# Kernel tuning notes

Measured on AMD Instinct MI355X. Metric: run time of the kernel, lower is better.

The kernel has to match this reference:

```python
import jax, jax.numpy as jnp
import numpy as np

N = 4  # hypercomplex dimension

def setup_inputs() -> dict:
    key = jax.random.key(0)
    k1, k2, k3 = jax.random.split(key, 3)
    x = jax.random.normal(k1, (32, 196, 768), dtype=jnp.float32)
    # [n, out_pad/n, in_pad/n] = [4, 3072//4, 768//4]
    weight_components = jax.random.normal(k2, (N, 768, 192), dtype=jnp.float32) * 0.02
    bias = jax.random.normal(k3, (3072,), dtype=jnp.float32) * 0.02
    return {"x": x, "weight_components": weight_components, "bias": bias}

def reference(x, weight_components, bias):
    n, out_blk, in_blk = weight_components.shape
    batch_shape = x.shape[:-1]
    xb = x.reshape(-1, n, in_blk)  # [B, n, in_blk]
    # original: out[:, (i+j)%n] += x[:, j] @ W[i].T
    # equivalently out[:, k] = sum_j x[:, j] @ W[(k-j)%n].T
    k_idx = jnp.arange(n)[:, None]
    j_idx = jnp.arange(n)[None, :]
    Wperm = weight_components[(k_idx - j_idx) % n]  # [n(k), n(j), out_blk, in_blk]
    out = jnp.einsum('bjc,kjoc->bko', xb, Wperm)    # [B, n, out_blk]
    out = out.reshape(-1, n * out_blk) + bias
    return out.reshape(*batch_shape, n * out_blk)
```

## Files before the change

### kernel.cpp

```cpp
#include <hip/hip_runtime.h>
#include <stdint.h>

#define M_ROWS 6272
#define K_DIM  768
#define N_DIM  3072
#define BM 128
#define BN 128
#define BK 32
#define NITER (K_DIM / BK)

#define X_CHUNKS (M_ROWS * K_DIM / 8)
#define W_CHUNKS (N_DIM * K_DIM / 8)
#define X_BLOCKS (X_CHUNKS / 256)
#define W_BLOCKS (W_CHUNKS / 256)

typedef unsigned short u16;
typedef __attribute__((ext_vector_type(8))) __bf16 bf16x8;
typedef __attribute__((ext_vector_type(4))) float f32x4;

__device__ __forceinline__ u16 f32_to_bf16(float f) {
    unsigned u = __float_as_uint(f);
    unsigned r = 0x7FFFu + ((u >> 16) & 1u);
    return (u16)((u + r) >> 16);
}

__device__ __forceinline__ unsigned pack2(float a, float b) {
    return (unsigned)f32_to_bf16(a) | ((unsigned)f32_to_bf16(b) << 16);
}

__global__ void prep_kernel(const float* __restrict__ x, const float* __restrict__ w,
                            u16* __restrict__ xb, u16* __restrict__ wb) {
    int b = blockIdx.x;
    if (b < X_BLOCKS) {
        int idx = b * 256 + threadIdx.x;
        const float4* xp = (const float4*)x + (size_t)idx * 2;
        float4 a = xp[0], c = xp[1];
        uint4 v;
        v.x = pack2(a.x, a.y);
        v.y = pack2(a.z, a.w);
        v.z = pack2(c.x, c.y);
        v.w = pack2(c.z, c.w);
        ((uint4*)xb)[idx] = v;
    } else {
        int idx = (b - X_BLOCKS) * 256 + threadIdx.x;
        int n    = idx / 96;
        int kc   = idx - n * 96;
        int kblk = n / 768;
        int o    = n - kblk * 768;
        int j    = kc / 24;
        int c8   = kc - j * 24;
        int i    = (kblk - j) & 3;
        const float* src = w + (((size_t)i * 768 + o) * 192 + c8 * 8);
        float4 a = ((const float4*)src)[0];
        float4 c = ((const float4*)src)[1];
        uint4 v;
        v.x = pack2(a.x, a.y);
        v.y = pack2(a.z, a.w);
        v.z = pack2(c.x, c.y);
        v.w = pack2(c.z, c.w);
        ((uint4*)wb)[idx] = v;
    }
}

__device__ __forceinline__ void load_lds16(const u16* g, u16* l) {
    __builtin_amdgcn_global_load_lds(
        (const __attribute__((address_space(1))) void*)g,
        (__attribute__((address_space(3))) void*)l, 16, 0, 0);
}

__global__ __launch_bounds__(256) void gemm_bt(
    const u16* __restrict__ A,
    const u16* __restrict__ B,
    const float* __restrict__ bias,
    float* __restrict__ C)
{
    __shared__ u16 As[2][BM * BK];
    __shared__ u16 Bs[2][BN * BK];

    const int tid    = threadIdx.x;
    const int wave   = tid >> 6;
    const int lane   = tid & 63;
    const int lane16 = lane & 15;
    const int quad   = lane >> 4;
    const int wr     = wave >> 1;
    const int wc     = wave & 1;

    const int rowBase = blockIdx.y * BM;
    const int colBase = blockIdx.x * BN;

    const int c0 = tid;
    const int c1 = tid + 256;
    const int r0 = c0 >> 2, s0 = (c0 & 3) ^ ((r0 >> 1) & 3);
    const int r1 = c1 >> 2, s1 = (c1 & 3) ^ ((r1 >> 1) & 3);
    const u16* Ag0 = A + (size_t)(rowBase + r0) * K_DIM + s0 * 8;
    const u16* Ag1 = A + (size_t)(rowBase + r1) * K_DIM + s1 * 8;
    const u16* Bg0 = B + (size_t)(colBase + r0) * K_DIM + s0 * 8;
    const u16* Bg1 = B + (size_t)(colBase + r1) * K_DIM + s1 * 8;
    const int l0 = c0 * 8;
    const int l1 = c1 * 8;

    const int swz  = (lane16 >> 1) & 3;
    const int slot = (quad ^ swz) * 8;
    int aoff[4], boff[4];
#pragma unroll
    for (int i = 0; i < 4; ++i)
        aoff[i] = (wr * 64 + i * 16 + lane16) * BK + slot;
#pragma unroll
    for (int j = 0; j < 4; ++j)
        boff[j] = (wc * 64 + j * 16 + lane16) * BK + slot;

    f32x4 acc[4][4] = {};

    load_lds16(Ag0, &As[0][l0]);
    load_lds16(Ag1, &As[0][l1]);
    load_lds16(Bg0, &Bs[0][l0]);
    load_lds16(Bg1, &Bs[0][l1]);

#pragma unroll 2
    for (int it = 0; it < NITER; ++it) {
        const int cur = it & 1, nxt = cur ^ 1;
        __syncthreads();
        if (it + 1 < NITER) {
            const int k = (it + 1) * BK;
            load_lds16(Ag0 + k, &As[nxt][l0]);
            load_lds16(Ag1 + k, &As[nxt][l1]);
            load_lds16(Bg0 + k, &Bs[nxt][l0]);
            load_lds16(Bg1 + k, &Bs[nxt][l1]);
        }

        bf16x8 af[4], bfv[4];
#pragma unroll
        for (int i = 0; i < 4; ++i)
            af[i] = *(const bf16x8*)&As[cur][aoff[i]];
#pragma unroll
        for (int j = 0; j < 4; ++j)
            bfv[j] = *(const bf16x8*)&Bs[cur][boff[j]];
#pragma unroll
        for (int i = 0; i < 4; ++i)
#pragma unroll
            for (int j = 0; j < 4; ++j)
                acc[i][j] = __builtin_amdgcn_mfma_f32_16x16x32_bf16(
                    af[i], bfv[j], acc[i][j], 0, 0, 0);
    }

    float bv[4];
#pragma unroll
    for (int j = 0; j < 4; ++j)
        bv[j] = bias[colBase + wc * 64 + j * 16 + lane16];
#pragma unroll
    for (int i = 0; i < 4; ++i) {
        int row0 = rowBase + wr * 64 + i * 16 + quad * 4;
#pragma unroll
        for (int r = 0; r < 4; ++r) {
            float* cp = C + (size_t)(row0 + r) * N_DIM + colBase + wc * 64 + lane16;
#pragma unroll
            for (int j = 0; j < 4; ++j)
                cp[j * 16] = acc[i][j][r] + bv[j];
        }
    }
}

extern "C" void kernel_launch(void* const* d_in, const int* in_sizes, int n_in,
                              void* d_out, int out_size, void* d_ws, size_t ws_size,
                              hipStream_t stream) {
    const float* x    = (const float*)d_in[0];
    const float* w    = (const float*)d_in[1];
    const float* bias = (const float*)d_in[2];
    float* out = (float*)d_out;

    u16* xb = (u16*)d_ws;
    u16* wb = (u16*)((char*)d_ws + (size_t)M_ROWS * K_DIM * 2);

    hipLaunchKernelGGL(prep_kernel, dim3(X_BLOCKS + W_BLOCKS), dim3(256),
                       0, stream, x, w, xb, wb);
    hipLaunchKernelGGL(gemm_bt, dim3(N_DIM / BN, M_ROWS / BM), dim3(256),
                       0, stream, xb, wb, bias, out);
}
```

Before: 140.0 us.

## Replace direct global-to-LDS loads with register-staged double-buffered prefetch

Stops using global_load_lds direct-to-LDS copies and instead loads each tile into registers two iterations ahead, writing them into the other LDS buffer after the MFMA block. The main loop is restructured with a prologue and two peeled epilogue iterations, with one barrier per iteration placed after the stores. The aim is to hide global-load latency behind the MFMA work. In exchange it uses more VGPRs and adds an extra LDS write instruction per chunk.

```diff
diff --git a/kernel.cpp b/kernel.cpp
--- a/kernel.cpp
+++ b/kernel.cpp
@@ -62,12 +62,6 @@
     }
 }
 
-__device__ __forceinline__ void load_lds16(const u16* g, u16* l) {
-    __builtin_amdgcn_global_load_lds(
-        (const __attribute__((address_space(1))) void*)g,
-        (__attribute__((address_space(3))) void*)l, 16, 0, 0);
-}
-
 __global__ __launch_bounds__(256) void gemm_bt(
     const u16* __restrict__ A,
     const u16* __restrict__ B,
@@ -92,12 +86,15 @@
     const int c1 = tid + 256;
     const int r0 = c0 >> 2, s0 = (c0 & 3) ^ ((r0 >> 1) & 3);
     const int r1 = c1 >> 2, s1 = (c1 & 3) ^ ((r1 >> 1) & 3);
-    const u16* Ag0 = A + (size_t)(rowBase + r0) * K_DIM + s0 * 8;
-    const u16* Ag1 = A + (size_t)(rowBase + r1) * K_DIM + s1 * 8;
-    const u16* Bg0 = B + (size_t)(colBase + r0) * K_DIM + s0 * 8;
-    const u16* Bg1 = B + (size_t)(colBase + r1) * K_DIM + s1 * 8;
-    const int l0 = c0 * 8;
-    const int l1 = c1 * 8;
+    const uint4* Ag0 = (const uint4*)(A + (size_t)(rowBase + r0) * K_DIM + s0 * 8);
+    const uint4* Ag1 = (const uint4*)(A + (size_t)(rowBase + r1) * K_DIM + s1 * 8);
+    const uint4* Bg0 = (const uint4*)(B + (size_t)(colBase + r0) * K_DIM + s0 * 8);
+    const uint4* Bg1 = (const uint4*)(B + (size_t)(colBase + r1) * K_DIM + s1 * 8);
+    uint4* Al0 = (uint4*)&As[0][c0 * 8];
+    uint4* Al1 = (uint4*)&As[0][c1 * 8];
+    uint4* Bl0 = (uint4*)&Bs[0][c0 * 8];
+    uint4* Bl1 = (uint4*)&Bs[0][c1 * 8];
+    const int bufStride = (BM * BK) / 8;
 
     const int swz  = (lane16 >> 1) & 3;
     const int slot = (quad ^ swz) * 8;
@@ -111,23 +108,60 @@
 
     f32x4 acc[4][4] = {};
 
-    load_lds16(Ag0, &As[0][l0]);
-    load_lds16(Ag1, &As[0][l1]);
-    load_lds16(Bg0, &Bs[0][l0]);
-    load_lds16(Bg1, &Bs[0][l1]);
+    const int kStep = BK / 8;
+
+    uint4 ga0 = Ag0[0], ga1 = Ag1[0], gb0 = Bg0[0], gb1 = Bg1[0];
+    Al0[0] = ga0; Al1[0] = ga1; Bl0[0] = gb0; Bl1[0] = gb1;
+    ga0 = Ag0[kStep]; ga1 = Ag1[kStep]; gb0 = Bg0[kStep]; gb1 = Bg1[kStep];
+    __syncthreads();
 
 #pragma unroll 2
-    for (int it = 0; it < NITER; ++it) {
+    for (int it = 0; it < NITER - 2; ++it) {
         const int cur = it & 1, nxt = cur ^ 1;
+
+        bf16x8 af[4], bfv[4];
+#pragma unroll
+        for (int i = 0; i < 4; ++i)
+            af[i] = *(const bf16x8*)&As[cur][aoff[i]];
+#pragma unroll
+        for (int j = 0; j < 4; ++j)
+            bfv[j] = *(const bf16x8*)&Bs[cur][boff[j]];
+#pragma unroll
+        for (int i = 0; i < 4; ++i)
+#pragma unroll
+            for (int j = 0; j < 4; ++j)
+                acc[i][j] = __builtin_amdgcn_mfma_f32_16x16x32_bf16(
+                    af[i], bfv[j], acc[i][j], 0, 0, 0);
+
+        const int o = nxt * bufStride;
+        Al0[o] = ga0; Al1[o] = ga1; Bl0[o] = gb0; Bl1[o] = gb1;
+        const int g = (it + 2) * kStep;
+        ga0 = Ag0[g]; ga1 = Ag1[g]; gb0 = Bg0[g]; gb1 = Bg1[g];
         __syncthreads();
-        if (it + 1 < NITER) {
-            const int k = (it + 1) * BK;
-            load_lds16(Ag0 + k, &As[nxt][l0]);
-            load_lds16(Ag1 + k, &As[nxt][l1]);
-            load_lds16(Bg0 + k, &Bs[nxt][l0]);
-            load_lds16(Bg1 + k, &Bs[nxt][l1]);
-        }
-
+    }
+
+    {
+        const int cur = (NITER - 2) & 1, nxt = cur ^ 1;
+        bf16x8 af[4], bfv[4];
+#pragma unroll
+        for (int i = 0; i < 4; ++i)
+            af[i] = *(const bf16x8*)&As[cur][aoff[i]];
+#pragma unroll
+        for (int j = 0; j < 4; ++j)
+            bfv[j] = *(const bf16x8*)&Bs[cur][boff[j]];
+#pragma unroll
+        for (int i = 0; i < 4; ++i)
+#pragma unroll
+            for (int j = 0; j < 4; ++j)
+                acc[i][j] = __builtin_amdgcn_mfma_f32_16x16x32_bf16(
+                    af[i], bfv[j], acc[i][j], 0, 0, 0);
+        const int o = nxt * bufStride;
+        Al0[o] = ga0; Al1[o] = ga1; Bl0[o] = gb0; Bl1[o] = gb1;
+        __syncthreads();
+    }
+
+    {
+        const int cur = (NITER - 1) & 1;
         bf16x8 af[4], bfv[4];
 #pragma unroll
         for (int i = 0; i < 4; ++i)
```

Result: faster. 134.9 us (-3.7%).

## Load GEMM operand fragments directly from global memory into registers, bypassing LDS

Applied to the files above, without the earlier changes.

Removes the shared-memory double buffer and block-wide barriers. Each wave loads its A and B MFMA fragments directly from global memory into registers, with one-iteration register prefetch. This cuts LDS traffic and synchronisation but loses intra-block data sharing, doubling global/L2 reads, and the per-lane strided row accesses may coalesce poorly.

```diff
diff --git a/kernel.cpp b/kernel.cpp
--- a/kernel.cpp
+++ b/kernel.cpp
@@ -4,10 +4,7 @@
 #define M_ROWS 6272
 #define K_DIM  768
 #define N_DIM  3072
-#define BM 128
-#define BN 128
-#define BK 32
-#define NITER (K_DIM / BK)
+#define NITER (K_DIM / 32)
 
 #define X_CHUNKS (M_ROWS * K_DIM / 8)
 #define W_CHUNKS (N_DIM * K_DIM / 8)
@@ -62,21 +59,12 @@
     }
 }
 
-__device__ __forceinline__ void load_lds16(const u16* g, u16* l) {
-    __builtin_amdgcn_global_load_lds(
-        (const __attribute__((address_space(1))) void*)g,
-        (__attribute__((address_space(3))) void*)l, 16, 0, 0);
-}
-
 __global__ __launch_bounds__(256) void gemm_bt(
     const u16* __restrict__ A,
     const u16* __restrict__ B,
     const float* __restrict__ bias,
     float* __restrict__ C)
 {
-    __shared__ u16 As[2][BM * BK];
-    __shared__ u16 Bs[2][BN * BK];
-
     const int tid    = threadIdx.x;
     const int wave   = tid >> 6;
     const int lane   = tid & 63;
@@ -85,74 +73,55 @@
     const int wr     = wave >> 1;
     const int wc     = wave & 1;
 
-    const int rowBase = blockIdx.y * BM;
-    const int colBase = blockIdx.x * BN;
+    const int rowBase = blockIdx.y * 128 + wr * 64;
+    const int colBase = blockIdx.x * 128 + wc * 64;
 
-    const int c0 = tid;
-    const int c1 = tid + 256;
-    const int r0 = c0 >> 2, s0 = (c0 & 3) ^ ((r0 >> 1) & 3);
-    const int r1 = c1 >> 2, s1 = (c1 & 3) ^ ((r1 >> 1) & 3);
-    const u16* Ag0 = A + (size_t)(rowBase + r0) * K_DIM + s0 * 8;
-    const u16* Ag1 = A + (size_t)(rowBase + r1) * K_DIM + s1 * 8;
-    const u16* Bg0 = B + (size_t)(colBase + r0) * K_DIM + s0 * 8;
-    const u16* Bg1 = B + (size_t)(colBase + r1) * K_DIM + s1 * 8;
-    const int l0 = c0 * 8;
-    const int l1 = c1 * 8;
-
-    const int swz  = (lane16 >> 1) & 3;
-    const int slot = (quad ^ swz) * 8;
-    int aoff[4], boff[4];
+    const u16* ap[4];
+    const u16* bp[4];
 #pragma unroll
     for (int i = 0; i < 4; ++i)
-        aoff[i] = (wr * 64 + i * 16 + lane16) * BK + slot;
+        ap[i] = A + (size_t)(rowBase + i * 16 + lane16) * K_DIM + quad * 8;
 #pragma unroll
     for (int j = 0; j < 4; ++j)
-        boff[j] = (wc * 64 + j * 16 + lane16) * BK + slot;
+        bp[j] = B + (size_t)(colBase + j * 16 + lane16) * K_DIM + quad * 8;
 
     f32x4 acc[4][4] = {};
 
-    load_lds16(Ag0, &As[0][l0]);
-    load_lds16(Ag1, &As[0][l1]);
-    load_lds16(Bg0, &Bs[0][l0]);
-    load_lds16(Bg1, &Bs[0][l1]);
+    bf16x8 a0[4], b0[4], a1[4], b1[4];
+#pragma unroll
+    for (int i = 0; i < 4; ++i) a0[i] = *(const bf16x8*)(ap[i]);
+#pragma unroll
+    for (int j = 0; j < 4; ++j) b0[j] = *(const bf16x8*)(bp[j]);
 
 #pragma unroll 2
     for (int it = 0; it < NITER; ++it) {
-        const int cur = it & 1, nxt = cur ^ 1;
-        __syncthreads();
         if (it + 1 < NITER) {
-            const int k = (it + 1) * BK;
-            load_lds16(Ag0 + k, &As[nxt][l0]);
-            load_lds16(Ag1 + k, &As[nxt][l1]);
-            load_lds16(Bg0 + k, &Bs[nxt][l0]);
-            load_lds16(Bg1 + k, &Bs[nxt][l1]);
+            const int k = (it + 1) * 32;
+#pragma unroll
+            for (int i = 0; i < 4; ++i) a1[i] = *(const bf16x8*)(ap[i] + k);
+#pragma unroll
+            for (int j = 0; j < 4; ++j) b1[j] = *(const bf16x8*)(bp[j] + k);
         }
-
-        bf16x8 af[4], bfv[4];
-#pragma unroll
-        for (int i = 0; i < 4; ++i)
-            af[i] = *(const bf16x8*)&As[cur][aoff[i]];
-#pragma unroll
-        for (int j = 0; j < 4; ++j)
-            bfv[j] = *(const bf16x8*)&Bs[cur][boff[j]];
 #pragma unroll
         for (int i = 0; i < 4; ++i)
 #pragma unroll
             for (int j = 0; j < 4; ++j)
                 acc[i][j] = __builtin_amdgcn_mfma_f32_16x16x32_bf16(
-                    af[i], bfv[j], acc[i][j], 0, 0, 0);
+                    a0[i], b0[j], acc[i][j], 0, 0, 0);
+#pragma unroll
+        for (int i = 0; i < 4; ++i) { a0[i] = a1[i]; b0[i] = b1[i]; }
     }
 
     float bv[4];
 #pragma unroll
     for (int j = 0; j < 4; ++j)
-        bv[j] = bias[colBase + wc * 64 + j * 16 + lane16];
+        bv[j] = bias[colBase + j * 16 + lane16];
 #pragma unroll
     for (int i = 0; i < 4; ++i) {
-        int row0 = rowBase + wr * 64 + i * 16 + quad * 4;
+        int row0 = rowBase + i * 16 + quad * 4;
 #pragma unroll
         for (int r = 0; r < 4; ++r) {
-            float* cp = C + (size_t)(row0 + r) * N_DIM + colBase + wc * 64 + lane16;
+            float* cp = C + (size_t)(row0 + r) * N_DIM + colBase + lane16;
 #pragma unroll
             for (int j = 0; j < 4; ++j)
                 cp[j * 16] = acc[i][j][r] + bv[j];
@@ -173,6 +142,6 @@
 
     hipLaunchKernelGGL(prep_kernel, dim3(X_BLOCKS + W_BLOCKS), dim3(256),
                        0, stream, x, w, xb, wb);
-    hipLaunchKernelGGL(gemm_bt, dim3(N_DIM / BN, M_ROWS / BM), dim3(256),
+    hipLaunchKernelGGL(gemm_bt, dim3(N_DIM / 128, M_ROWS / 128), dim3(256),
                        0, stream, xb, wb, bias, out);
 }
```

Result: slower. 201.0 us (+43.5%).
